# Optimization experiments

Measured on AMD Instinct MI355X. Metric: run time of the kernel, lower is better.

Reference implementation:

```python
import jax, jax.numpy as jnp
import numpy as np

N, E, C, NE, G, T = 20000, 320000, 32, 10, 64, 1000
NB, HID, LAYERS = 8, 64, 2
R_MAX, P_CUT, AVG_NEIGH = 5.0, 6, 16.0
LM = 16  # (max_ell+1)^2 spherical-harmonic components
L_OF_LM = jnp.array([0,1,1,1,2,2,2,2,2,3,3,3,3,3,3,3])


def sph_harm(u):
    # component-normalized real spherical harmonics up to l=3 on unit vectors u [E,3]
    x, y, z = u[:, 0], u[:, 1], u[:, 2]
    s3, s15, s5, s105, s7 = 3**0.5, 15**0.5, 5**0.5, 105**0.5, 7**0.5
    s35_8, s21_8 = (35.0/8.0)**0.5, (21.0/8.0)**0.5
    comps = [jnp.ones_like(x),
             s3*x, s3*y, s3*z,
             s15*x*y, s15*y*z, 0.5*s5*(3*z*z-1.0), s15*x*z, 0.5*s15*(x*x-y*y),
             s35_8*y*(3*x*x-y*y), s105*x*y*z, s21_8*y*(5*z*z-1.0),
             0.5*s7*(5*z*z*z-3*z), s21_8*x*(5*z*z-1.0),
             0.5*s105*z*(x*x-y*y), s35_8*x*(x*x-3*y*y)]
    return jnp.stack(comps, axis=-1)  # [E,16]


def radial_embed(r):
    # Bessel basis with polynomial cutoff (MACE RadialEmbeddingBlock)
    n = jnp.arange(1, NB + 1, dtype=r.dtype)
    rc = jnp.maximum(r, 1e-9)
    bessel = (2.0/R_MAX)**0.5 * jnp.sin(n[None, :]*jnp.pi*rc[:, None]/R_MAX) / rc[:, None]
    xr = r / R_MAX
    p = float(P_CUT)
    f = (1.0 - 0.5*(p+1)*(p+2)*xr**p + p*(p+2)*xr**(p+1) - 0.5*p*(p+1)*xr**(p+2))
    f = f * (xr < 1.0)
    return bessel * f[:, None]  # [E,NB]


def setup_inputs():
    key = jax.random.key(0)
    ks = jax.random.split(key, 16)
    positions = jax.random.normal(ks[0], (N, 3)) * 3.0
    species = jax.random.randint(ks[1], (N,), 0, NE)
    node_attrs = jax.nn.one_hot(species, NE, dtype=jnp.float32)
    edge_index = jax.random.randint(ks[2], (2, E), 0, N)
    shifts = jnp.zeros((E, 3), jnp.float32)
    batch = jnp.sort(jax.random.randint(ks[3], (N,), 0, G))
    t = jax.random.randint(ks[4], (G,), 0, T)
    eps = jax.random.normal(ks[5], (N, NE + 3))
    betas = jnp.linspace(1e-4, 0.02, T)
    alpha_bar = jnp.cumprod(1.0 - betas)
    sc = 0.1
    W_embed = sc * jax.random.normal(ks[6], (NE + 1, C))
    W_r1 = sc * jax.random.normal(ks[7], (LAYERS, NB, HID))
    W_r2 = sc * jax.random.normal(ks[8], (LAYERS, HID, C * 4))
    W_mix = sc * jax.random.normal(ks[9], (LAYERS, 4, C, C))
    W_sc = sc * jax.random.normal(ks[10], (NE, C))
    W_prod = sc * jax.random.normal(ks[11], (LAYERS, 3, C))
    W_ro_s = sc * jax.random.normal(ks[12], (LAYERS, C, NE))
    W_ro_v = sc * jax.random.normal(ks[13], (LAYERS, C))
    return {"positions": positions, "node_attrs": node_attrs, "shifts": shifts,
            "eps": eps, "alpha_bar": alpha_bar, "W_embed": W_embed, "W_r1": W_r1,
            "W_r2": W_r2, "W_mix": W_mix, "W_sc": W_sc, "W_prod": W_prod,
            "W_ro_s": W_ro_s, "W_ro_v": W_ro_v, "edge_index": edge_index,
            "batch": batch, "t": t}


def reference(positions, node_attrs, shifts, eps, alpha_bar, W_embed, W_r1, W_r2,
              W_mix, W_sc, W_prod, W_ro_s, W_ro_v, edge_index, batch, t):
    sender, receiver = edge_index[0], edge_index[1]
    # diffusion: noise positions and attrs (DDPM q(x_t|x_0))
    ab = alpha_bar[t][batch][:, None]                       # [N,1]
    attrs0 = node_attrs / 4.0
    pos_noisy = jnp.sqrt(ab) * positions + jnp.sqrt(1.0 - ab) * eps[:, -3:]
    attrs_noisy = jnp.sqrt(ab) * attrs0 + jnp.sqrt(1.0 - ab) * eps[:, :NE]
    tf = (t.astype(jnp.float32) / T)[batch][:, None]
    h = jnp.concatenate([attrs_noisy, tf], axis=-1) @ W_embed  # [N,C]
    # edge geometry
    vec = pos_noisy[receiver] - pos_noisy[sender] + shifts
    r = jnp.sqrt(jnp.sum(vec * vec, axis=-1) + 1e-12)
    Y = sph_harm(vec / r[:, None])                          # [E,16]
    ef = radial_embed(r)                                    # [E,NB]
    scalar = h
    pred = jnp.zeros((N, NE + 3), h.dtype)
    for layer in range(LAYERS):
        rw = jax.nn.silu(ef @ W_r1[layer]) @ W_r2[layer]    # [E,4C]
        rw = rw.reshape(E, C, 4)[:, :, L_OF_LM]             # [E,C,16]
        msg = rw * scalar[sender][:, :, None] * Y[:, None, :]
        agg = jax.ops.segment_sum(msg, receiver, num_segments=N) / AVG_NEIGH
        Wm = W_mix[layer][L_OF_LM]                          # [16,C,C]
        feats = jnp.einsum('nck,kcd->ndk', agg, Wm)         # per-l channel mix
        s = feats[:, :, 0]
        poly = W_prod[layer, 0] + W_prod[layer, 1] * s + W_prod[layer, 2] * s * s
        feats = feats * poly[:, :, None]                    # correlation-3 product
        if layer == 0:
            feats = feats.at[:, :, 0].add(attrs_noisy @ W_sc)  # element skip
        scalar = feats[:, :, 0]
        pred_s = scalar @ W_ro_s[layer]                     # [N,NE]
        pred_v = jnp.einsum('ncm,c->nm', feats[:, :, 1:4], W_ro_v[layer])  # [N,3]
        pred = pred + jnp.concatenate([pred_s, pred_v], axis=-1)
    err = (pred - eps) ** 2
    loss_pos = jax.ops.segment_sum(err[:, -3:].sum(-1), batch, num_segments=G)
    loss_lab = jax.ops.segment_sum(err[:, :NE].sum(-1), batch, num_segments=G)
    nn = jax.ops.segment_sum(jnp.ones((N,), pred.dtype), batch, num_segments=G)
    loss = 0.5 * (loss_pos + loss_lab) / (jnp.maximum(nn, 1.0) * (3 + NE))
    return loss
```

## Files before the change

### kernel.cpp

```cpp
#include <hip/hip_runtime.h>

typedef unsigned short ushort_t;
typedef unsigned int uint_t;

#define NN 20000
#define EE 320000
#define CC 32
#define NEL 10
#define GG 64
#define TTT 1000
#define NBB 8
#define HIDD 64
#define EPB 256

typedef __attribute__((ext_vector_type(8))) short bf16x8;
typedef __attribute__((ext_vector_type(4))) float f32x4;

__device__ __forceinline__ float bits2f(uint_t b) { union { uint_t u; float f; } v; v.u = b; return v.f; }
__device__ __forceinline__ ushort_t f2b(float f) {
  union { float f; uint_t u; } v; v.f = f;
  uint_t r = (v.u + 0x7fffu + ((v.u >> 16) & 1u)) >> 16;
  return (ushort_t)r;
}
__device__ __forceinline__ uint_t pk(float a, float b) {
  return (uint_t)f2b(a) | ((uint_t)f2b(b) << 16);
}
__device__ __forceinline__ float lo16(uint_t u) { return bits2f(u << 16); }
__device__ __forceinline__ float hi16(uint_t u) { return bits2f(u & 0xffff0000u); }

__global__ __launch_bounds__(256) void k_prep(
    const float* __restrict__ positions, const float* __restrict__ node_attrs,
    const float* __restrict__ eps, const float* __restrict__ alpha_bar,
    const float* __restrict__ W_embed, const float* __restrict__ W_sc,
    const int* __restrict__ batch, const int* __restrict__ tarr,
    float* __restrict__ pos_noisy, float* __restrict__ scalA,
    float* __restrict__ sc_skip, float* __restrict__ pred, int* __restrict__ deg)
{
  int n = blockIdx.x * 256 + threadIdx.x;
  if (n >= NN) return;
  deg[n] = 0;
  int g = batch[n];
  int tn = tarr[g];
  float ab = alpha_bar[tn];
  float sa = sqrtf(ab), sb = sqrtf(fmaxf(1.0f - ab, 0.0f));
#pragma unroll
  for (int j = 0; j < 3; ++j)
    pos_noisy[n * 3 + j] = sa * positions[n * 3 + j] + sb * eps[n * 13 + 10 + j];
  float an[10];
#pragma unroll
  for (int j = 0; j < 10; ++j)
    an[j] = sa * 0.25f * node_attrs[n * 10 + j] + sb * eps[n * 13 + j];
  float tf = (float)tn * (1.0f / (float)TTT);
  for (int d = 0; d < CC; ++d) {
    float h = tf * W_embed[10 * CC + d];
    float sk = 0.0f;
#pragma unroll
    for (int j = 0; j < 10; ++j) {
      h = fmaf(an[j], W_embed[j * CC + d], h);
      sk = fmaf(an[j], W_sc[j * CC + d], sk);
    }
    scalA[n * CC + d] = h;
    sc_skip[n * CC + d] = sk;
  }
#pragma unroll
  for (int j = 0; j < 13; ++j) pred[n * 13 + j] = 0.0f;
}

__global__ __launch_bounds__(256) void k_edge_deg(const int* __restrict__ ei,
    int* __restrict__ deg)
{
  int e = blockIdx.x * 256 + threadIdx.x;
  atomicAdd(&deg[ei[EE + e]], 1);
}

__global__ __launch_bounds__(1024) void k_scan(const int* __restrict__ deg,
    int* __restrict__ offs, int* __restrict__ cursor,
    float* __restrict__ lnum, float* __restrict__ lcnt)
{
  __shared__ int wsums[16];
  __shared__ int woffs[16];
  int tid = threadIdx.x, lane = tid & 63, wv = tid >> 6;
  if (tid < GG) { lnum[tid] = 0.0f; lcnt[tid] = 0.0f; }
  int base = tid * 20;
  int loc[20];
  int s = 0;
#pragma unroll
  for (int j = 0; j < 20; ++j) {
    int idx = base + j;
    int v = (idx < NN) ? deg[idx] : 0;
    loc[j] = s; s += v;
  }
  int inc = s;
  for (int o = 1; o < 64; o <<= 1) {
    int v = __shfl_up(inc, o, 64);
    if (lane >= o) inc += v;
  }
  if (lane == 63) wsums[wv] = inc;
  __syncthreads();
  if (wv == 0 && lane < 16) {
    int v = wsums[lane];
    int i2 = v;
    for (int o = 1; o < 16; o <<= 1) {
      int vv = __shfl_up(i2, o, 16);
      if (lane >= o) i2 += vv;
    }
    woffs[lane] = i2 - v;
  }
  __syncthreads();
  int texcl = woffs[wv] + (inc - s);
#pragma unroll
  for (int j = 0; j < 20; ++j) {
    int idx = base + j;
    if (idx < NN) { int v = texcl + loc[j]; offs[idx] = v; cursor[idx] = v; }
  }
  if (tid == 1023) offs[NN] = EE;
}

__global__ __launch_bounds__(256) void k_edge2(
    const float* __restrict__ pos_noisy, const float* __restrict__ shifts,
    const int* __restrict__ ei, int* __restrict__ cursor,
    ushort_t* __restrict__ Ys, ushort_t* __restrict__ efs, int* __restrict__ snds)
{
  int e = blockIdx.x * 256 + threadIdx.x;
  int snd = ei[e], rcv = ei[EE + e];
  float vx = pos_noisy[rcv * 3 + 0] - pos_noisy[snd * 3 + 0] + shifts[e * 3 + 0];
  float vy = pos_noisy[rcv * 3 + 1] - pos_noisy[snd * 3 + 1] + shifts[e * 3 + 1];
  float vz = pos_noisy[rcv * 3 + 2] - pos_noisy[snd * 3 + 2] + shifts[e * 3 + 2];
  float r2 = vx * vx + vy * vy + vz * vz + 1e-12f;
  float r = sqrtf(r2);
  float inv = 1.0f / r;
  float x = vx * inv, y = vy * inv, z = vz * inv;

  const float s3 = 1.7320508075688772f, s15 = 3.872983346207417f, s5 = 2.23606797749979f;
  const float s105 = 10.246950765959598f, s7 = 2.6457513110645907f;
  const float s35_8 = 2.091650066335189f, s21_8 = 1.6201851746019651f;
  float yv[16];
  yv[0] = 1.0f;
  yv[1] = s3 * x; yv[2] = s3 * y; yv[3] = s3 * z;
  yv[4] = s15 * x * y;
  yv[5] = s15 * y * z;
  yv[6] = 0.5f * s5 * (3.0f * z * z - 1.0f);
  yv[7] = s15 * x * z;
  yv[8] = 0.5f * s15 * (x * x - y * y);
  yv[9] = s35_8 * y * (3.0f * x * x - y * y);
  yv[10] = s105 * x * y * z;
  yv[11] = s21_8 * y * (5.0f * z * z - 1.0f);
  yv[12] = 0.5f * s7 * (5.0f * z * z * z - 3.0f * z);
  yv[13] = s21_8 * x * (5.0f * z * z - 1.0f);
  yv[14] = 0.5f * s105 * z * (x * x - y * y);
  yv[15] = s35_8 * x * (x * x - 3.0f * y * y);

  float rc = fmaxf(r, 1e-9f);
  float pref = 0.6324555320336759f / rc;
  float th = 0.6283185307179586f * rc;
  float s1 = __sinf(th), c1 = __cosf(th);
  float xr = r * 0.2f;
  float fcut = 0.0f;
  if (xr < 1.0f) {
    float x2 = xr * xr, x3 = x2 * xr;
    float x6 = x3 * x3, x7 = x6 * xr, x8 = x7 * xr;
    fcut = 1.0f - 28.0f * x6 + 48.0f * x7 - 21.0f * x8;
  }
  float efv[8];
  float sp = 0.0f, scur = s1, c2 = 2.0f * c1;
#pragma unroll
  for (int b = 0; b < 8; ++b) {
    efv[b] = pref * scur * fcut;
    float nx = c2 * scur - sp;
    sp = scur; scur = nx;
  }

  int slot = atomicAdd(&cursor[rcv], 1);
  snds[slot] = snd;
  uint4* Y4 = (uint4*)Ys;
  Y4[(size_t)slot * 2 + 0] = make_uint4(pk(yv[0], yv[1]), pk(yv[2], yv[3]),
                                        pk(yv[4], yv[5]), pk(yv[6], yv[7]));
  Y4[(size_t)slot * 2 + 1] = make_uint4(pk(yv[8], yv[9]), pk(yv[10], yv[11]),
                                        pk(yv[12], yv[13]), pk(yv[14], yv[15]));
  ((uint4*)efs)[slot] = make_uint4(pk(efv[0], efv[1]), pk(efv[2], efv[3]),
                                   pk(efv[4], efv[5]), pk(efv[6], efv[7]));
}

__global__ __launch_bounds__(256) void k_rw_mfma(
    const ushort_t* __restrict__ efs, const float* __restrict__ W_r1,
    const float* __restrict__ W_r2, const int* __restrict__ snds,
    const float* __restrict__ scal_in, ushort_t* __restrict__ rwc, int layer)
{
  __shared__ __align__(16) ushort_t w2t[128][72];
  __shared__ __align__(16) ushort_t h1[EPB][72];
  int tid = threadIdx.x;
  const float* W1g = W_r1 + layer * NBB * HIDD;
  const float* W2g = W_r2 + layer * HIDD * 128;
  for (int idx = tid; idx < HIDD * 128; idx += 256) {
    int k = idx >> 7, n = idx & 127;
    w2t[n][k] = f2b(W2g[idx]);
  }
  {
    int e = blockIdx.x * EPB + tid;
    uint4 q = ((const uint4*)efs)[e];
    float efr[8] = {lo16(q.x), hi16(q.x), lo16(q.y), hi16(q.y),
                    lo16(q.z), hi16(q.z), lo16(q.w), hi16(q.w)};
    for (int hc = 0; hc < 8; ++hc) {
      float v[8];
#pragma unroll
      for (int hh = 0; hh < 8; ++hh) {
        int h = hc * 8 + hh;
        float t = 0.0f;
#pragma unroll
        for (int b = 0; b < 8; ++b) t = fmaf(efr[b], W1g[b * HIDD + h], t);
        v[hh] = t / (1.0f + __expf(-t));
      }
      *(uint4*)&h1[tid][hc * 8] = make_uint4(pk(v[0], v[1]), pk(v[2], v[3]),
                                             pk(v[4], v[5]), pk(v[6], v[7]));
    }
  }
  __syncthreads();
  int w = tid >> 6, lane = tid & 63;
  int c = lane & 15, quad = lane >> 4;
  bf16x8 bfr[16];
#pragma unroll
  for (int nt = 0; nt < 8; ++nt)
#pragma unroll
    for (int kt = 0; kt < 2; ++kt)
      bfr[nt * 2 + kt] = *(const bf16x8*)&w2t[nt * 16 + c][kt * 32 + quad * 8];
  int mb0 = w * 64;
#pragma unroll
  for (int mt = 0; mt < 4; ++mt) {
    int mbase = mb0 + mt * 16;
    bf16x8 a0 = *(const bf16x8*)&h1[mbase + c][quad * 8];
    bf16x8 a1 = *(const bf16x8*)&h1[mbase + c][32 + quad * 8];
    size_t erow = (size_t)blockIdx.x * EPB + mbase + quad * 4;
    int4 sn = *(const int4*)&snds[erow];
    const float* sb0 = scal_in + (size_t)sn.x * CC;
    const float* sb1 = scal_in + (size_t)sn.y * CC;
    const float* sb2 = scal_in + (size_t)sn.z * CC;
    const float* sb3 = scal_in + (size_t)sn.w * CC;
#pragma unroll
    for (int nt = 0; nt < 8; ++nt) {
      f32x4 acc = {0.0f, 0.0f, 0.0f, 0.0f};
      acc = __builtin_amdgcn_mfma_f32_16x16x32_bf16(a0, bfr[nt * 2 + 0], acc, 0, 0, 0);
      acc = __builtin_amdgcn_mfma_f32_16x16x32_bf16(a1, bfr[nt * 2 + 1], acc, 0, 0, 0);
      int col = nt * 16 + c;
      int cc = col >> 2;
      rwc[(erow + 0) * 128 + col] = f2b(acc[0] * sb0[cc]);
      rwc[(erow + 1) * 128 + col] = f2b(acc[1] * sb1[cc]);
      rwc[(erow + 2) * 128 + col] = f2b(acc[2] * sb2[cc]);
      rwc[(erow + 3) * 128 + col] = f2b(acc[3] * sb3[cc]);
    }
  }
}

__global__ __launch_bounds__(256) void k_layer(
    const ushort_t* __restrict__ Ys, const ushort_t* __restrict__ rwc,
    float* __restrict__ scal_out,
    const int* __restrict__ offs,
    const float* __restrict__ W_mix, const float* __restrict__ W_prod,
    const float* __restrict__ W_ro_s, const float* __restrict__ W_ro_v,
    const float* __restrict__ sc_skip, float* __restrict__ pred, int layer)
{
  __shared__ float lagg[4][CC][16];
  __shared__ float lf[4][CC][4];
  int w = threadIdx.x >> 6, lane = threadIdx.x & 63;
  int n = blockIdx.x * 4 + w;
  int c = lane >> 1;
  int kh = lane & 1;
  int kb = kh * 8;
  int i0 = offs[n], i1 = offs[n + 1];
  float acc0 = 0, acc1 = 0, acc2 = 0, acc3 = 0, acc4 = 0, acc5 = 0, acc6 = 0, acc7 = 0;
  const uint4* Y4 = (const uint4*)Ys;
  const uint2* rw2 = (const uint2*)rwc;
  int s = i0;
  for (; s + 2 <= i1; s += 2) {
    uint4 qa = Y4[(size_t)s * 2 + kh];
    uint2 ra = rw2[(size_t)s * 32 + c];
    uint4 qb = Y4[(size_t)(s + 1) * 2 + kh];
    uint2 rb = rw2[(size_t)(s + 1) * 32 + c];
    {
      float r0 = lo16(ra.x), r1 = hi16(ra.x), r2v = lo16(ra.y), r3 = hi16(ra.y);
      float w0 = kh ? r2v : r0, w13 = kh ? r3 : r1, w47 = kh ? r3 : r2v;
      acc0 = fmaf(w0,  lo16(qa.x), acc0);
      acc1 = fmaf(w13, hi16(qa.x), acc1);
      acc2 = fmaf(w13, lo16(qa.y), acc2);
      acc3 = fmaf(w13, hi16(qa.y), acc3);
      acc4 = fmaf(w47, lo16(qa.z), acc4);
      acc5 = fmaf(w47, hi16(qa.z), acc5);
      acc6 = fmaf(w47, lo16(qa.w), acc6);
      acc7 = fmaf(w47, hi16(qa.w), acc7);
    }
    {
      float r0 = lo16(rb.x), r1 = hi16(rb.x), r2v = lo16(rb.y), r3 = hi16(rb.y);
      float w0 = kh ? r2v : r0, w13 = kh ? r3 : r1, w47 = kh ? r3 : r2v;
      acc0 = fmaf(w0,  lo16(qb.x), acc0);
      acc1 = fmaf(w13, hi16(qb.x), acc1);
      acc2 = fmaf(w13, lo16(qb.y), acc2);
      acc3 = fmaf(w13, hi16(qb.y), acc3);
      acc4 = fmaf(w47, lo16(qb.z), acc4);
      acc5 = fmaf(w47, hi16(qb.z), acc5);
      acc6 = fmaf(w47, lo16(qb.w), acc6);
      acc7 = fmaf(w47, hi16(qb.w), acc7);
    }
  }
  if (s < i1) {
    uint4 q = Y4[(size_t)s * 2 + kh];
    uint2 rp = rw2[(size_t)s * 32 + c];
    float r0 = lo16(rp.x), r1 = hi16(rp.x), r2v = lo16(rp.y), r3 = hi16(rp.y);
    float w0 = kh ? r2v : r0, w13 = kh ? r3 : r1, w47 = kh ? r3 : r2v;
    acc0 = fmaf(w0,  lo16(q.x), acc0);
    acc1 = fmaf(w13, hi16(q.x), acc1);
    acc2 = fmaf(w13, lo16(q.y), acc2);
    acc3 = fmaf(w13, hi16(q.y), acc3);
    acc4 = fmaf(w47, lo16(q.z), acc4);
    acc5 = fmaf(w47, hi16(q.z), acc5);
    acc6 = fmaf(w47, lo16(q.w), acc6);
    acc7 = fmaf(w47, hi16(q.w), acc7);
  }
  const float invavg = 1.0f / 16.0f;
  lagg[w][c][kb + 0] = acc0 * invavg;
  lagg[w][c][kb + 1] = acc1 * invavg;
  lagg[w][c][kb + 2] = acc2 * invavg;
  lagg[w][c][kb + 3] = acc3 * invavg;
  lagg[w][c][kb + 4] = acc4 * invavg;
  lagg[w][c][kb + 5] = acc5 * invavg;
  lagg[w][c][kb + 6] = acc6 * invavg;
  lagg[w][c][kb + 7] = acc7 * invavg;
  __syncthreads();
  int d = c;
  float ft[8] = {0, 0, 0, 0, 0, 0, 0, 0};
  const float* Wm = W_mix + layer * 4096;
  for (int cc2 = 0; cc2 < CC; ++cc2) {
    float m0 = Wm[cc2 * CC + d];
    float m1 = Wm[1024 + cc2 * CC + d];
    float m2 = Wm[2048 + cc2 * CC + d];
    float m3 = Wm[3072 + cc2 * CC + d];
    float u0 = kh ? m2 : m0;
    float u13 = kh ? m3 : m1;
    float u47 = kh ? m3 : m2;
    ft[0] = fmaf(lagg[w][cc2][kb + 0], u0, ft[0]);
    ft[1] = fmaf(lagg[w][cc2][kb + 1], u13, ft[1]);
    ft[2] = fmaf(lagg[w][cc2][kb + 2], u13, ft[2]);
    ft[3] = fmaf(lagg[w][cc2][kb + 3], u13, ft[3]);
    ft[4] = fmaf(lagg[w][cc2][kb + 4], u47, ft[4]);
    ft[5] = fmaf(lagg[w][cc2][kb + 5], u47, ft[5]);
    ft[6] = fmaf(lagg[w][cc2][kb + 6], u47, ft[6]);
    ft[7] = fmaf(lagg[w][cc2][kb + 7], u47, ft[7]);
  }
  float sv = __shfl(ft[0], lane & 62, 64);
  const float* Wp = W_prod + layer * 96;
  float p0 = Wp[d], p1 = Wp[32 + d], p2 = Wp[64 + d];
  float poly = fmaf(fmaf(p2, sv, p1), sv, p0);
#pragma unroll
  for (int j = 0; j < 8; ++j) ft[j] *= poly;
  if (layer == 0 && kh == 0) ft[0] += sc_skip[n * CC + d];
  if (kh == 0) {
    scal_out[n * CC + d] = ft[0];
    lf[w][d][0] = ft[0]; lf[w][d][1] = ft[1]; lf[w][d][2] = ft[2]; lf[w][d][3] = ft[3];
  }
  __syncthreads();
  if (lane < 13) {
    float sum = 0.0f;
    if (lane < 10) {
      const float* Wr = W_ro_s + layer * CC * NEL;
      for (int dd = 0; dd < CC; ++dd) sum = fmaf(lf[w][dd][0], Wr[dd * NEL + lane], sum);
    } else {
      int mm = lane - 10;
      const float* Wv = W_ro_v + layer * CC;
      for (int dd = 0; dd < CC; ++dd) sum = fmaf(lf[w][dd][1 + mm], Wv[dd], sum);
    }
    pred[n * 13 + lane] += sum;
  }
}

__global__ __launch_bounds__(256) void k_loss(const float* __restrict__ pred,
    const float* __restrict__ eps, const int* __restrict__ batch,
    float* __restrict__ lnum, float* __restrict__ lcnt)
{
  __shared__ float psum[GG];
  __shared__ int pcnt[GG];
  int tid = threadIdx.x;
  if (tid < GG) { psum[tid] = 0.0f; pcnt[tid] = 0; }
  __syncthreads();
  int n = blockIdx.x * 256 + tid;
  if (n < NN) {
    int g = batch[n];
    float sum = 0.0f;
#pragma unroll
    for (int j = 0; j < 13; ++j) {
      float dlt = pred[n * 13 + j] - eps[n * 13 + j];
      sum = fmaf(dlt, dlt, sum);
    }
    atomicAdd(&psum[g], sum);
    atomicAdd(&pcnt[g], 1);
  }
  __syncthreads();
  if (tid < GG && pcnt[tid] > 0) {
    atomicAdd(&lnum[tid], psum[tid]);
    atomicAdd(&lcnt[tid], (float)pcnt[tid]);
  }
}

__global__ void k_final(const float* __restrict__ lnum, const float* __restrict__ lcnt,
    float* __restrict__ out)
{
  int g = threadIdx.x;
  if (g < GG) {
    float nn = fmaxf(lcnt[g], 1.0f);
    out[g] = 0.5f * lnum[g] / (nn * 13.0f);
  }
}

extern "C" void kernel_launch(void* const* d_in, const int* in_sizes, int n_in,
                              void* d_out, int out_size, void* d_ws, size_t ws_size,
                              hipStream_t stream) {
  const float* positions  = (const float*)d_in[0];
  const float* node_attrs = (const float*)d_in[1];
  const float* shifts     = (const float*)d_in[2];
  const float* eps        = (const float*)d_in[3];
  const float* alpha_bar  = (const float*)d_in[4];
  const float* W_embed    = (const float*)d_in[5];
  const float* W_r1       = (const float*)d_in[6];
  const float* W_r2       = (const float*)d_in[7];
  const float* W_mix      = (const float*)d_in[8];
  const float* W_sc       = (const float*)d_in[9];
  const float* W_prod     = (const float*)d_in[10];
  const float* W_ro_s     = (const float*)d_in[11];
  const float* W_ro_v     = (const float*)d_in[12];
  const int* edge_index   = (const int*)d_in[13];
  const int* batch        = (const int*)d_in[14];
  const int* tarr         = (const int*)d_in[15];
  float* out = (float*)d_out;

  char* ws = (char*)d_ws;
  size_t off = 0;
  auto alloc = [&](size_t bytes) -> void* {
    void* p = ws + off;
    off = (off + bytes + 255) & ~(size_t)255;
    return p;
  };
  float* pos_noisy = (float*)alloc(NN * 3 * 4);
  float* scalA     = (float*)alloc(NN * CC * 4);
  float* scalB     = (float*)alloc(NN * CC * 4);
  float* sc_skip   = (float*)alloc(NN * CC * 4);
  float* pred      = (float*)alloc(NN * 13 * 4);
  ushort_t* Ys     = (ushort_t*)alloc((size_t)EE * 16 * 2);
  ushort_t* efs    = (ushort_t*)alloc((size_t)EE * 8 * 2);
  int* snds        = (int*)alloc((size_t)EE * 4);
  ushort_t* rwc    = (ushort_t*)alloc((size_t)EE * 128 * 2);
  int* deg         = (int*)alloc(NN * 4);
  int* offs        = (int*)alloc((NN + 1) * 4);
  int* cursor      = (int*)alloc(NN * 4);
  float* lnum      = (float*)alloc(GG * 4);
  float* lcnt      = (float*)alloc(GG * 4);
  (void)ws_size; (void)in_sizes; (void)n_in; (void)out_size;

  const int NB_N = (NN + 255) / 256;
  const int NB_E = EE / 256;

  k_prep<<<NB_N, 256, 0, stream>>>(positions, node_attrs, eps, alpha_bar, W_embed,
                                   W_sc, batch, tarr, pos_noisy, scalA, sc_skip, pred, deg);
  k_edge_deg<<<NB_E, 256, 0, stream>>>(edge_index, deg);
  k_scan<<<1, 1024, 0, stream>>>(deg, offs, cursor, lnum, lcnt);
  k_edge2<<<NB_E, 256, 0, stream>>>(pos_noisy, shifts, edge_index, cursor, Ys, efs, snds);

  for (int layer = 0; layer < 2; ++layer) {
    const float* sin_p = (layer == 0) ? scalA : scalB;
    float* sout_p      = (layer == 0) ? scalB : scalA;
    k_rw_mfma<<<NB_E, 256, 0, stream>>>(efs, W_r1, W_r2, snds, sin_p, rwc, layer);
    k_layer<<<NN / 4, 256, 0, stream>>>(Ys, rwc, sout_p, offs,
                                        W_mix, W_prod, W_ro_s, W_ro_v,
                                        sc_skip, pred, layer);
  }

  k_loss<<<NB_N, 256, 0, stream>>>(pred, eps, batch, lnum, lcnt);
  k_final<<<1, 64, 0, stream>>>(lnum, lcnt, out);
}
```

Baseline: 341.6 us.

## Transpose radial MFMA for packed stores, unroll gather loop, fuse final loss

```diff
diff --git a/kernel.cpp b/kernel.cpp
--- a/kernel.cpp
+++ b/kernel.cpp
@@ -11,7 +11,7 @@
 #define TTT 1000
 #define NBB 8
 #define HIDD 64
-#define EPB 256
+#define EPB 128
 
 typedef __attribute__((ext_vector_type(8))) short bf16x8;
 typedef __attribute__((ext_vector_type(4))) float f32x4;
@@ -75,12 +75,13 @@
 
 __global__ __launch_bounds__(1024) void k_scan(const int* __restrict__ deg,
     int* __restrict__ offs, int* __restrict__ cursor,
-    float* __restrict__ lnum, float* __restrict__ lcnt)
+    float* __restrict__ lnum, float* __restrict__ lcnt, int* __restrict__ ticket)
 {
   __shared__ int wsums[16];
   __shared__ int woffs[16];
   int tid = threadIdx.x, lane = tid & 63, wv = tid >> 6;
   if (tid < GG) { lnum[tid] = 0.0f; lcnt[tid] = 0.0f; }
+  if (tid == 64) *ticket = 0;
   int base = tid * 20;
   int loc[20];
   int s = 0;
@@ -181,13 +182,14 @@
                                    pk(efv[4], efv[5]), pk(efv[6], efv[7]));
 }
 
-__global__ __launch_bounds__(256) void k_rw_mfma(
+__global__ __launch_bounds__(256) void k_rw2(
     const ushort_t* __restrict__ efs, const float* __restrict__ W_r1,
     const float* __restrict__ W_r2, const int* __restrict__ snds,
     const float* __restrict__ scal_in, ushort_t* __restrict__ rwc, int layer)
 {
   __shared__ __align__(16) ushort_t w2t[128][72];
-  __shared__ __align__(16) ushort_t h1[EPB][72];
+  __shared__ __align__(16) ushort_t h1t[EPB][72];
+  __shared__ __align__(16) float w1s[NBB * HIDD];
   int tid = threadIdx.x;
   const float* W1g = W_r1 + layer * NBB * HIDD;
   const float* W2g = W_r2 + layer * HIDD * 128;
@@ -195,57 +197,56 @@
     int k = idx >> 7, n = idx & 127;
     w2t[n][k] = f2b(W2g[idx]);
   }
+  for (int i = tid; i < NBB * HIDD; i += 256) w1s[i] = W1g[i];
+  __syncthreads();
   {
-    int e = blockIdx.x * EPB + tid;
-    uint4 q = ((const uint4*)efs)[e];
-    float efr[8] = {lo16(q.x), hi16(q.x), lo16(q.y), hi16(q.y),
+    int e = tid & 127, half = tid >> 7;
+    uint4 q = ((const uint4*)efs)[(size_t)blockIdx.x * EPB + e];
+    float ef8[8] = {lo16(q.x), hi16(q.x), lo16(q.y), hi16(q.y),
                     lo16(q.z), hi16(q.z), lo16(q.w), hi16(q.w)};
-    for (int hc = 0; hc < 8; ++hc) {
+    for (int hc = 0; hc < 4; ++hc) {
       float v[8];
 #pragma unroll
       for (int hh = 0; hh < 8; ++hh) {
-        int h = hc * 8 + hh;
+        int h = half * 32 + hc * 8 + hh;
         float t = 0.0f;
 #pragma unroll
-        for (int b = 0; b < 8; ++b) t = fmaf(efr[b], W1g[b * HIDD + h], t);
+        for (int b = 0; b < 8; ++b) t = fmaf(ef8[b], w1s[b * HIDD + h], t);
         v[hh] = t / (1.0f + __expf(-t));
       }
-      *(uint4*)&h1[tid][hc * 8] = make_uint4(pk(v[0], v[1]), pk(v[2], v[3]),
-                                             pk(v[4], v[5]), pk(v[6], v[7]));
+      *(uint4*)&h1t[e][half * 32 + hc * 8] =
+          make_uint4(pk(v[0], v[1]), pk(v[2], v[3]), pk(v[4], v[5]), pk(v[6], v[7]));
     }
   }
   __syncthreads();
   int w = tid >> 6, lane = tid & 63;
-  int c = lane & 15, quad = lane >> 4;
-  bf16x8 bfr[16];
-#pragma unroll
-  for (int nt = 0; nt < 8; ++nt)
-#pragma unroll
-    for (int kt = 0; kt < 2; ++kt)
-      bfr[nt * 2 + kt] = *(const bf16x8*)&w2t[nt * 16 + c][kt * 32 + quad * 8];
-  int mb0 = w * 64;
-#pragma unroll
-  for (int mt = 0; mt < 4; ++mt) {
-    int mbase = mb0 + mt * 16;
-    bf16x8 a0 = *(const bf16x8*)&h1[mbase + c][quad * 8];
-    bf16x8 a1 = *(const bf16x8*)&h1[mbase + c][32 + quad * 8];
-    size_t erow = (size_t)blockIdx.x * EPB + mbase + quad * 4;
-    int4 sn = *(const int4*)&snds[erow];
-    const float* sb0 = scal_in + (size_t)sn.x * CC;
-    const float* sb1 = scal_in + (size_t)sn.y * CC;
-    const float* sb2 = scal_in + (size_t)sn.z * CC;
-    const float* sb3 = scal_in + (size_t)sn.w * CC;
+  int c16 = lane & 15, quad = lane >> 4;
+  bf16x8 afr[16];
+#pragma unroll
+  for (int nt = 0; nt < 8; ++nt) {
+    afr[nt * 2 + 0] = *(const bf16x8*)&w2t[nt * 16 + c16][quad * 8];
+    afr[nt * 2 + 1] = *(const bf16x8*)&w2t[nt * 16 + c16][32 + quad * 8];
+  }
+#pragma unroll
+  for (int mt = 0; mt < 2; ++mt) {
+    int mbase = w * 32 + mt * 16;
+    bf16x8 b0 = *(const bf16x8*)&h1t[mbase + c16][quad * 8];
+    bf16x8 b1 = *(const bf16x8*)&h1t[mbase + c16][32 + quad * 8];
+    size_t eg = (size_t)blockIdx.x * EPB + mbase + c16;
+    int snd = snds[eg];
+    const float* sb = scal_in + (size_t)snd * CC + quad;
+    float ssv[8];
+#pragma unroll
+    for (int nt = 0; nt < 8; ++nt) ssv[nt] = sb[nt * 4];
+    uint2* dst = (uint2*)(rwc + eg * 128);
 #pragma unroll
     for (int nt = 0; nt < 8; ++nt) {
       f32x4 acc = {0.0f, 0.0f, 0.0f, 0.0f};
-      acc = __builtin_amdgcn_mfma_f32_16x16x32_bf16(a0, bfr[nt * 2 + 0], acc, 0, 0, 0);
-      acc = __builtin_amdgcn_mfma_f32_16x16x32_bf16(a1, bfr[nt * 2 + 1], acc, 0, 0, 0);
-      int col = nt * 16 + c;
-      int cc = col >> 2;
-      rwc[(erow + 0) * 128 + col] = f2b(acc[0] * sb0[cc]);
-      rwc[(erow + 1) * 128 + col] = f2b(acc[1] * sb1[cc]);
-      rwc[(erow + 2) * 128 + col] = f2b(acc[2] * sb2[cc]);
-      rwc[(erow + 3) * 128 + col] = f2b(acc[3] * sb3[cc]);
+      acc = __builtin_amdgcn_mfma_f32_16x16x32_bf16(afr[nt * 2 + 0], b0, acc, 0, 0, 0);
+      acc = __builtin_amdgcn_mfma_f32_16x16x32_bf16(afr[nt * 2 + 1], b1, acc, 0, 0, 0);
+      float s = ssv[nt];
+      dst[nt * 4 + quad] = make_uint2(pk(acc[0] * s, acc[1] * s),
+                                      pk(acc[2] * s, acc[3] * s));
     }
   }
 }
@@ -270,37 +271,32 @@
   const uint4* Y4 = (const uint4*)Ys;
   const uint2* rw2 = (const uint2*)rwc;
   int s = i0;
-  for (; s + 2 <= i1; s += 2) {
-    uint4 qa = Y4[(size_t)s * 2 + kh];
-    uint2 ra = rw2[(size_t)s * 32 + c];
-    uint4 qb = Y4[(size_t)(s + 1) * 2 + kh];
-    uint2 rb = rw2[(size_t)(s + 1) * 32 + c];
-    {
-      float r0 = lo16(ra.x), r1 = hi16(ra.x), r2v = lo16(ra.y), r3 = hi16(ra.y);
+  for (; s + 4 <= i1; s += 4) {
+    uint4 q0 = Y4[(size_t)(s + 0) * 2 + kh];
+    uint2 p0 = rw2[(size_t)(s + 0) * 32 + c];
+    uint4 q1 = Y4[(size_t)(s + 1) * 2 + kh];
+    uint2 p1 = rw2[(size_t)(s + 1) * 32 + c];
+    uint4 q2 = Y4[(size_t)(s + 2) * 2 + kh];
+    uint2 p2 = rw2[(size_t)(s + 2) * 32 + c];
+    uint4 q3 = Y4[(size_t)(s + 3) * 2 + kh];
+    uint2 p3 = rw2[(size_t)(s + 3) * 32 + c];
+#pragma unroll
+    for (int u = 0; u < 4; ++u) {
+      uint4 q = (u == 0) ? q0 : (u == 1) ? q1 : (u == 2) ? q2 : q3;
+      uint2 rp = (u == 0) ? p0 : (u == 1) ? p1 : (u == 2) ? p2 : p3;
+      float r0 = lo16(rp.x), r1 = hi16(rp.x), r2v = lo16(rp.y), r3 = hi16(rp.y);
       float w0 = kh ? r2v : r0, w13 = kh ? r3 : r1, w47 = kh ? r3 : r2v;
-      acc0 = fmaf(w0,  lo16(qa.x), acc0);
-      acc1 = fmaf(w13, hi16(qa.x), acc1);
-      acc2 = fmaf(w13, lo16(qa.y), acc2);
-      acc3 = fmaf(w13, hi16(qa.y), acc3);
-      acc4 = fmaf(w47, lo16(qa.z), acc4);
-      acc5 = fmaf(w47, hi16(qa.z), acc5);
-      acc6 = fmaf(w47, lo16(qa.w), acc6);
-      acc7 = fmaf(w47, hi16(qa.w), acc7);
-    }
-    {
-      float r0 = lo16(rb.x), r1 = hi16(rb.x), r2v = lo16(rb.y), r3 = hi16(rb.y);
-      float w0 = kh ? r2v : r0, w13 = kh ? r3 : r1, w47 = kh ? r3 : r2v;
-      acc0 = fmaf(w0,  lo16(qb.x), acc0);
-      acc1 = fmaf(w13, hi16(qb.x), acc1);
-      acc2 = fmaf(w13, lo16(qb.y), acc2);
-      acc3 = fmaf(w13, hi16(qb.y), acc3);
-      acc4 = fmaf(w47, lo16(qb.z), acc4);
-      acc5 = fmaf(w47, hi16(qb.z), acc5);
-      acc6 = fmaf(w47, lo16(qb.w), acc6);
-      acc7 = fmaf(w47, hi16(qb.w), acc7);
-    }
-  }
-  if (s < i1) {
+      acc0 = fmaf(w0,  lo16(q.x), acc0);
+      acc1 = fmaf(w13, hi16(q.x), acc1);
+      acc2 = fmaf(w13, lo16(q.y), acc2);
+      acc3 = fmaf(w13, hi16(q.y), acc3);
+      acc4 = fmaf(w47, lo16(q.z), acc4);
+      acc5 = fmaf(w47, hi16(q.z), acc5);
+      acc6 = fmaf(w47, lo16(q.w), acc6);
+      acc7 = fmaf(w47, hi16(q.w), acc7);
+    }
+  }
+  for (; s < i1; ++s) {
     uint4 q = Y4[(size_t)s * 2 + kh];
     uint2 rp = rw2[(size_t)s * 32 + c];
     float r0 = lo16(rp.x), r1 = hi16(rp.x), r2v = lo16(rp.y), r3 = hi16(rp.y);
@@ -372,10 +368,12 @@
 
 __global__ __launch_bounds__(256) void k_loss(const float* __restrict__ pred,
     const float* __restrict__ eps, const int* __restrict__ batch,
-    float* __restrict__ lnum, float* __restrict__ lcnt)
+    float* __restrict__ lnum, float* __restrict__ lcnt,
+    int* __restrict__ ticket, float* __restrict__ out, int nblocks)
 {
   __shared__ float psum[GG];
   __shared__ int pcnt[GG];
+  __shared__ int lastflag;
   int tid = threadIdx.x;
   if (tid < GG) { psum[tid] = 0.0f; pcnt[tid] = 0; }
   __syncthreads();
@@ -396,15 +394,17 @@
     atomicAdd(&lnum[tid], psum[tid]);
     atomicAdd(&lcnt[tid], (float)pcnt[tid]);
   }
-}
-
-__global__ void k_final(const float* __restrict__ lnum, const float* __restrict__ lcnt,
-    float* __restrict__ out)
-{
-  int g = threadIdx.x;
-  if (g < GG) {
-    float nn = fmaxf(lcnt[g], 1.0f);
-    out[g] = 0.5f * lnum[g] / (nn * 13.0f);
+  __syncthreads();
+  if (tid == 0) {
+    __threadfence();
+    int t = atomicAdd(ticket, 1);
+    lastflag = (t == nblocks - 1) ? 1 : 0;
+  }
+  __syncthreads();
+  if (lastflag && tid < GG) {
+    float num = atomicAdd(&lnum[tid], 0.0f);
+    float cnt = atomicAdd(&lcnt[tid], 0.0f);
+    out[tid] = 0.5f * num / (fmaxf(cnt, 1.0f) * 13.0f);
   }
 }
 
@@ -450,6 +450,7 @@
   int* cursor      = (int*)alloc(NN * 4);
   float* lnum      = (float*)alloc(GG * 4);
   float* lcnt      = (float*)alloc(GG * 4);
+  int* ticket      = (int*)alloc(4);
   (void)ws_size; (void)in_sizes; (void)n_in; (void)out_size;
 
   const int NB_N = (NN + 255) / 256;
@@ -458,18 +459,17 @@
   k_prep<<<NB_N, 256, 0, stream>>>(positions, node_attrs, eps, alpha_bar, W_embed,
                                    W_sc, batch, tarr, pos_noisy, scalA, sc_skip, pred, deg);
   k_edge_deg<<<NB_E, 256, 0, stream>>>(edge_index, deg);
-  k_scan<<<1, 1024, 0, stream>>>(deg, offs, cursor, lnum, lcnt);
+  k_scan<<<1, 1024, 0, stream>>>(deg, offs, cursor, lnum, lcnt, ticket);
   k_edge2<<<NB_E, 256, 0, stream>>>(pos_noisy, shifts, edge_index, cursor, Ys, efs, snds);
 
   for (int layer = 0; layer < 2; ++layer) {
     const float* sin_p = (layer == 0) ? scalA : scalB;
     float* sout_p      = (layer == 0) ? scalB : scalA;
-    k_rw_mfma<<<NB_E, 256, 0, stream>>>(efs, W_r1, W_r2, snds, sin_p, rwc, layer);
+    k_rw2<<<EE / EPB, 256, 0, stream>>>(efs, W_r1, W_r2, snds, sin_p, rwc, layer);
     k_layer<<<NN / 4, 256, 0, stream>>>(Ys, rwc, sout_p, offs,
                                         W_mix, W_prod, W_ro_s, W_ro_v,
                                         sc_skip, pred, layer);
   }
 
-  k_loss<<<NB_N, 256, 0, stream>>>(pred, eps, batch, lnum, lcnt);
-  k_final<<<1, 64, 0, stream>>>(lnum, lcnt, out);
-}
+  k_loss<<<NB_N, 256, 0, stream>>>(pred, eps, batch, lnum, lcnt, ticket, out, NB_N);
+}
```

New measurement: 354.8 us. 1.04x slower.
